# Kernel optimization log

Measured on AMD Instinct MI355X. Metric: run time of the kernel, lower is better.

The kernel has to match this reference:

```python
import jax, jax.numpy as jnp
import numpy as np


def setup_inputs() -> dict:
    key = jax.random.key(0)
    k1, k2 = jax.random.split(key)
    inputs = jax.random.normal(k1, (16, 64, 64, 512), dtype=jnp.float32)
    gamma = jax.random.normal(k2, (1,), dtype=jnp.float32)
    return {"inputs": inputs, "gamma": gamma}


def reference(inputs, gamma):
    # inputs: [B, H, W, C] (NHWC), gamma: [1]
    b, h, w, c = inputs.shape
    vec_a = inputs.reshape(b, h * w, c)           # [B, HW, C]
    # channel-channel Gram matrix: [B, C, C]
    aTa = jnp.einsum('bnc,bnd->bcd', vec_a, vec_a)
    softmax_aTa = jax.nn.softmax(aTa, axis=-1)     # softmax over last channel axis
    # attend over channels: [B, HW, C] @ [B, C, C] -> [B, HW, C]
    aaTa = jnp.einsum('bnc,bcd->bnd', vec_a, softmax_aTa)
    aaTa = aaTa.reshape(b, h, w, c)
    return gamma * aaTa + inputs
```

## Files before the change

kernel.cpp:

```cpp
#include <hip/hip_runtime.h>
#include <stdint.h>

#define BB 16
#define NN 4096
#define CC 512
#define PELEM ((size_t)BB * CC * CC)

typedef __attribute__((ext_vector_type(8))) short bf16x8;
typedef __attribute__((ext_vector_type(4))) float f32x4;

__device__ __forceinline__ unsigned short to_bf16(float f) {
  unsigned int u = __float_as_uint(f);
  u += 0x7fffu + ((u >> 16) & 1u);
  return (unsigned short)(u >> 16);
}
__device__ __forceinline__ float bf16_to_f32(unsigned short h) {
  return __uint_as_float(((unsigned int)h) << 16);
}

__device__ __forceinline__ void gload_lds16(const void* g, void* l) {
  __builtin_amdgcn_global_load_lds(
      (const __attribute__((address_space(1))) unsigned int*)g,
      (__attribute__((address_space(3))) unsigned int*)l, 16, 0, 0);
}

template <int RS, int KLEN>
__device__ __forceinline__ void nt_gemm(const unsigned short* __restrict__ aB,
                                        const unsigned short* __restrict__ bB,
                                        f32x4 acc[4][4],
                                        unsigned short* lA, unsigned short* lB) {
  const int tid  = threadIdx.x;
  const int wid  = tid >> 6;
  const int lane = tid & 63;
  const int wr   = (wid >> 1) * 64;
  const int wc   = (wid & 1) * 64;

  const f32x4 zero = {0.f, 0.f, 0.f, 0.f};
#pragma unroll
  for (int i = 0; i < 4; ++i)
#pragma unroll
    for (int j = 0; j < 4; ++j) acc[i][j] = zero;

  const int srow = lane >> 3;
  const int gsrc = (lane & 7) ^ srow;

#pragma unroll 1
  for (int k0 = 0; k0 < KLEN; k0 += 64) {
#pragma unroll
    for (int i = 0; i < 4; ++i) {
      const int issue = wid * 4 + i;
      const int row   = issue * 8 + srow;
      const size_t go = (size_t)row * RS + k0 + gsrc * 8;
      gload_lds16(aB + go, lA + issue * 512);
      gload_lds16(bB + go, lB + issue * 512);
    }
    __syncthreads();

#pragma unroll
    for (int s = 0; s < 2; ++s) {
      bf16x8 af[4], bfr[4];
#pragma unroll
      for (int mf = 0; mf < 4; ++mf) {
        const int row = wr + mf * 16 + (lane & 15);
        const int ch  = (s * 4 + (lane >> 4)) ^ (row & 7);
        af[mf] = *(const bf16x8*)(lA + row * 64 + ch * 8);
      }
#pragma unroll
      for (int nf = 0; nf < 4; ++nf) {
        const int row = wc + nf * 16 + (lane & 15);
        const int ch  = (s * 4 + (lane >> 4)) ^ (row & 7);
        bfr[nf] = *(const bf16x8*)(lB + row * 64 + ch * 8);
      }
#pragma unroll
      for (int mf = 0; mf < 4; ++mf)
#pragma unroll
        for (int nf = 0; nf < 4; ++nf)
          acc[mf][nf] = __builtin_amdgcn_mfma_f32_16x16x32_bf16(
              af[mf], bfr[nf], acc[mf][nf], 0, 0, 0);
    }
    __syncthreads();
  }
}

__global__ __launch_bounds__(256) void k_convert(const float* __restrict__ in,
                                                 unsigned short* __restrict__ a16,
                                                 unsigned short* __restrict__ at16) {
  __shared__ unsigned short lt[64][68];
  const int b  = blockIdx.y;
  const int tn = blockIdx.x >> 3, tc = blockIdx.x & 7;
  const int n0 = tn * 64, c0 = tc * 64;
  const float* src = in + ((size_t)b * NN + n0) * CC + c0;
  unsigned short* adst = a16 + ((size_t)b * NN + n0) * CC + c0;

#pragma unroll
  for (int i = 0; i < 4; ++i) {
    const int id = i * 256 + threadIdx.x;
    const int n = id >> 4, ch = id & 15;
    float4 v = *(const float4*)(src + (size_t)n * CC + ch * 4);
    ushort4 o;
    o.x = to_bf16(v.x); o.y = to_bf16(v.y); o.z = to_bf16(v.z); o.w = to_bf16(v.w);
    *(ushort4*)(adst + (size_t)n * CC + ch * 4) = o;
    lt[ch * 4 + 0][n] = o.x;
    lt[ch * 4 + 1][n] = o.y;
    lt[ch * 4 + 2][n] = o.z;
    lt[ch * 4 + 3][n] = o.w;
  }
  __syncthreads();
  unsigned short* tdst = at16 + ((size_t)b * CC + c0) * NN + n0;
#pragma unroll
  for (int i = 0; i < 4; ++i) {
    const int id = i * 256 + threadIdx.x;
    const int c = id >> 4, ch2 = id & 15;
    uint2 w = *(const uint2*)&lt[c][ch2 * 4];
    *(uint2*)(tdst + (size_t)c * NN + ch2 * 4) = w;
  }
}

__global__ __launch_bounds__(256) void k_gram(const unsigned short* __restrict__ at,
                                              float* __restrict__ parts) {
  __shared__ __align__(16) unsigned short lA[128 * 64];
  __shared__ __align__(16) unsigned short lB[128 * 64];
  const int bid  = blockIdx.x;
  const int work = (bid & 7) * 128 + (bid >> 3);
  const int b    = work >> 6;
  const int r    = work & 63;
  const int ks   = r >> 4;
  const int tile = r & 15;
  const int c0 = (tile & 3) * 128;
  const int d0 = (tile >> 2) * 128;
  const unsigned short* aB = at + ((size_t)b * CC + c0) * NN + ks * 1024;
  const unsigned short* bB = at + ((size_t)b * CC + d0) * NN + ks * 1024;
  f32x4 acc[4][4];
  nt_gemm<NN, 1024>(aB, bB, acc, lA, lB);

  const int lane = threadIdx.x & 63, wid = threadIdx.x >> 6;
  const int wr = (wid >> 1) * 64, wc = (wid & 1) * 64;
  float* gb = parts + (size_t)ks * PELEM + (size_t)b * CC * CC;
#pragma unroll
  for (int mf = 0; mf < 4; ++mf)
#pragma unroll
    for (int nf = 0; nf < 4; ++nf)
#pragma unroll
      for (int q = 0; q < 4; ++q) {
        const int row = c0 + wr + mf * 16 + (lane >> 4) * 4 + q;
        const int col = d0 + wc + nf * 16 + (lane & 15);
        gb[(size_t)row * CC + col] = acc[mf][nf][q];
      }
}

__global__ __launch_bounds__(256) void k_softmax(const float* __restrict__ parts,
                                                 unsigned short* __restrict__ st) {
  __shared__ unsigned short ls[32][512];
  const int b  = blockIdx.x >> 4;
  const int cb = blockIdx.x & 15;
  const int wid = threadIdx.x >> 6, lane = threadIdx.x & 63;

#pragma unroll 1
  for (int i = 0; i < 8; ++i) {
    const int rl = wid * 8 + i;
    const int c  = cb * 32 + rl;
    const int r7 = rl & 7;
    const float* base = parts + ((size_t)b * CC + c) * CC;
    float4 v0 = {0.f, 0.f, 0.f, 0.f}, v1 = {0.f, 0.f, 0.f, 0.f};
#pragma unroll
    for (int p = 0; p < 4; ++p) {
      float4 a = *(const float4*)(base + (size_t)p * PELEM + lane * 4);
      float4 bq = *(const float4*)(base + (size_t)p * PELEM + 256 + lane * 4);
      v0.x += a.x; v0.y += a.y; v0.z += a.z; v0.w += a.w;
      v1.x += bq.x; v1.y += bq.y; v1.z += bq.z; v1.w += bq.w;
    }
    float m = fmaxf(fmaxf(fmaxf(v0.x, v0.y), fmaxf(v0.z, v0.w)),
                    fmaxf(fmaxf(v1.x, v1.y), fmaxf(v1.z, v1.w)));
#pragma unroll
    for (int off = 32; off > 0; off >>= 1) m = fmaxf(m, __shfl_xor(m, off));
    float e0 = expf(v0.x - m), e1 = expf(v0.y - m), e2 = expf(v0.z - m), e3 = expf(v0.w - m);
    float e4 = expf(v1.x - m), e5 = expf(v1.y - m), e6 = expf(v1.z - m), e7 = expf(v1.w - m);
    float s = e0 + e1 + e2 + e3 + e4 + e5 + e6 + e7;
#pragma unroll
    for (int off = 32; off > 0; off >>= 1) s += __shfl_xor(s, off);
    const float pinv = 1.0f / s;
    ushort4 o0, o1;
    o0.x = to_bf16(e0 * pinv); o0.y = to_bf16(e1 * pinv);
    o0.z = to_bf16(e2 * pinv); o0.w = to_bf16(e3 * pinv);
    o1.x = to_bf16(e4 * pinv); o1.y = to_bf16(e5 * pinv);
    o1.z = to_bf16(e6 * pinv); o1.w = to_bf16(e7 * pinv);
    *(ushort4*)&ls[rl][(lane ^ r7) << 2]         = o0;
    *(ushort4*)&ls[rl][256 + ((lane ^ r7) << 2)] = o1;
  }
  __syncthreads();

#pragma unroll 1
  for (int i = 0; i < 2; ++i) {
    const int d = i * 256 + threadIdx.x;
    unsigned int u[16];
#pragma unroll
    for (int k = 0; k < 16; ++k) {
      const int c0i = 2 * k, c1i = 2 * k + 1;
      const unsigned int lo = ls[c0i][(((d >> 2) ^ (c0i & 7)) << 2) | (d & 3)];
      const unsigned int hi = ls[c1i][(((d >> 2) ^ (c1i & 7)) << 2) | (d & 3)];
      u[k] = lo | (hi << 16);
    }
    unsigned short* dst = st + ((size_t)b * CC + d) * CC + cb * 32;
    uint4 w0 = {u[0], u[1], u[2], u[3]};
    uint4 w1 = {u[4], u[5], u[6], u[7]};
    uint4 w2 = {u[8], u[9], u[10], u[11]};
    uint4 w3 = {u[12], u[13], u[14], u[15]};
    *(uint4*)(dst + 0)  = w0;
    *(uint4*)(dst + 8)  = w1;
    *(uint4*)(dst + 16) = w2;
    *(uint4*)(dst + 24) = w3;
  }
}

__global__ __launch_bounds__(256) void k_out(const unsigned short* __restrict__ a16,
                                             const unsigned short* __restrict__ st,
                                             const float* __restrict__ gammap,
                                             float* __restrict__ outp) {
  __shared__ __align__(16) unsigned short lA[128 * 64];
  __shared__ __align__(16) unsigned short lB[128 * 64];
  const int bid  = blockIdx.x;
  const int work = (bid & 7) * 256 + (bid >> 3);
  const int b    = work >> 7;
  const int r    = work & 127;
  const int nt   = r >> 5;
  const int mt   = r & 31;
  const int n0 = mt * 128, d0 = nt * 128;
  const unsigned short* aB = a16 + ((size_t)b * NN + n0) * CC;
  const unsigned short* bB = st + ((size_t)b * CC + d0) * CC;
  f32x4 acc[4][4];
  nt_gemm<CC, CC>(aB, bB, acc, lA, lB);

  const float g = gammap[0];
  const int lane = threadIdx.x & 63, wid = threadIdx.x >> 6;
  const int wr = (wid >> 1) * 64, wc = (wid & 1) * 64;
  const unsigned short* xr = a16 + ((size_t)b * NN + n0) * CC + d0;
  float* ob = outp + ((size_t)b * NN + n0) * CC + d0;
#pragma unroll
  for (int mf = 0; mf < 4; ++mf)
#pragma unroll
    for (int nf = 0; nf < 4; ++nf)
#pragma unroll
      for (int q = 0; q < 4; ++q) {
        const int row = wr + mf * 16 + (lane >> 4) * 4 + q;
        const int col = wc + nf * 16 + (lane & 15);
        const size_t off = (size_t)row * CC + col;
        ob[off] = fmaf(g, acc[mf][nf][q], bf16_to_f32(xr[off]));
      }
}

extern "C" void kernel_launch(void* const* d_in, const int* in_sizes, int n_in,
                              void* d_out, int out_size, void* d_ws, size_t ws_size,
                              hipStream_t stream) {
  const float* in    = (const float*)d_in[0];
  const float* gamma = (const float*)d_in[1];
  float* outp = (float*)d_out;

  unsigned short* a16  = (unsigned short*)d_ws;
  unsigned short* stb  = (unsigned short*)((char*)d_ws + ((size_t)64 << 20));
  unsigned short* at16 = (unsigned short*)d_out;
  float*          parts = (float*)((char*)d_out + ((size_t)64 << 20));

  k_convert<<<dim3(512, 16), 256, 0, stream>>>(in, a16, at16);
  k_gram<<<dim3(1024), 256, 0, stream>>>(at16, parts);
  k_softmax<<<dim3(256), 256, 0, stream>>>(parts, stb);
  k_out<<<dim3(2048), 256, 0, stream>>>(a16, stb, gamma, outp);
}
```

Before: 370.7 us.

## Double-buffer GEMM LDS tiles, exploit Gram symmetry, and vectorize transpose in convert

The shared NT GEMM now uses two LDS buffers so the next k-tile's global-to-LDS loads are issued before computing the current tile, overlapping memory with MFMA work. The Gram kernel computes only upper-triangular 128x128 tiles (10 of 16 per batch and k-split) and writes the mirrored tile through an LDS transpose, cutting Gram launches from 1024 to 640 blocks. The convert kernel is restructured so each thread transposes a 4x4 block in registers and writes wider LDS and global stores. Double buffering doubles LDS per block to 64KB, which may reduce occupancy, and the mirrored write adds extra stores and syncs.

```diff
diff --git a/kernel.cpp b/kernel.cpp
--- a/kernel.cpp
+++ b/kernel.cpp
@@ -28,7 +28,7 @@
 __device__ __forceinline__ void nt_gemm(const unsigned short* __restrict__ aB,
                                         const unsigned short* __restrict__ bB,
                                         f32x4 acc[4][4],
-                                        unsigned short* lA, unsigned short* lB) {
+                                        unsigned short* lds) {
   const int tid  = threadIdx.x;
   const int wid  = tid >> 6;
   const int lane = tid & 63;
@@ -43,19 +43,21 @@
 
   const int srow = lane >> 3;
   const int gsrc = (lane & 7) ^ srow;
-
-#pragma unroll 1
-  for (int k0 = 0; k0 < KLEN; k0 += 64) {
+  constexpr int NT = KLEN / 64;
+
+  auto stage = [&](int bf, int k0) {
 #pragma unroll
     for (int i = 0; i < 4; ++i) {
       const int issue = wid * 4 + i;
       const int row   = issue * 8 + srow;
       const size_t go = (size_t)row * RS + k0 + gsrc * 8;
-      gload_lds16(aB + go, lA + issue * 512);
-      gload_lds16(bB + go, lB + issue * 512);
-    }
-    __syncthreads();
-
+      gload_lds16(aB + go, lds + bf * 16384 + issue * 512);
+      gload_lds16(bB + go, lds + bf * 16384 + 8192 + issue * 512);
+    }
+  };
+  auto compute = [&](int bf) {
+    const unsigned short* lA = lds + bf * 16384;
+    const unsigned short* lB = lA + 8192;
 #pragma unroll
     for (int s = 0; s < 2; ++s) {
       bf16x8 af[4], bfr[4];
@@ -78,64 +80,86 @@
           acc[mf][nf] = __builtin_amdgcn_mfma_f32_16x16x32_bf16(
               af[mf], bfr[nf], acc[mf][nf], 0, 0, 0);
     }
+  };
+
+  stage(0, 0);
+  __syncthreads();
+  int cur = 0;
+#pragma unroll 1
+  for (int t = 0; t < NT; ++t) {
+    if (t + 1 < NT) stage(cur ^ 1, (t + 1) * 64);
+    compute(cur);
     __syncthreads();
+    cur ^= 1;
   }
 }
 
 __global__ __launch_bounds__(256) void k_convert(const float* __restrict__ in,
                                                  unsigned short* __restrict__ a16,
                                                  unsigned short* __restrict__ at16) {
-  __shared__ unsigned short lt[64][68];
+  __shared__ unsigned short lt[64 * 68];
   const int b  = blockIdx.y;
   const int tn = blockIdx.x >> 3, tc = blockIdx.x & 7;
   const int n0 = tn * 64, c0 = tc * 64;
-  const float* src = in + ((size_t)b * NN + n0) * CC + c0;
-  unsigned short* adst = a16 + ((size_t)b * NN + n0) * CC + c0;
-
-#pragma unroll
-  for (int i = 0; i < 4; ++i) {
-    const int id = i * 256 + threadIdx.x;
-    const int n = id >> 4, ch = id & 15;
-    float4 v = *(const float4*)(src + (size_t)n * CC + ch * 4);
-    ushort4 o;
-    o.x = to_bf16(v.x); o.y = to_bf16(v.y); o.z = to_bf16(v.z); o.w = to_bf16(v.w);
-    *(ushort4*)(adst + (size_t)n * CC + ch * 4) = o;
-    lt[ch * 4 + 0][n] = o.x;
-    lt[ch * 4 + 1][n] = o.y;
-    lt[ch * 4 + 2][n] = o.z;
-    lt[ch * 4 + 3][n] = o.w;
+  const int t   = threadIdx.x;
+  const int ctc = t & 15;
+  const int ntq = t >> 4;
+
+  const float* src = in + ((size_t)b * NN + n0 + 4 * ntq) * CC + c0 + 4 * ctc;
+  unsigned short* adst = a16 + ((size_t)b * NN + n0 + 4 * ntq) * CC + c0 + 4 * ctc;
+
+  unsigned short ob[4][4];
+#pragma unroll
+  for (int j = 0; j < 4; ++j) {
+    float4 v = *(const float4*)(src + (size_t)j * CC);
+    ob[j][0] = to_bf16(v.x); ob[j][1] = to_bf16(v.y);
+    ob[j][2] = to_bf16(v.z); ob[j][3] = to_bf16(v.w);
+    ushort4 o = {ob[j][0], ob[j][1], ob[j][2], ob[j][3]};
+    *(ushort4*)(adst + (size_t)j * CC) = o;
+  }
+#pragma unroll
+  for (int q = 0; q < 4; ++q) {
+    ushort4 w = {ob[0][q], ob[1][q], ob[2][q], ob[3][q]};
+    *(ushort4*)&lt[(4 * ctc + q) * 68 + 4 * ntq] = w;
   }
   __syncthreads();
-  unsigned short* tdst = at16 + ((size_t)b * CC + c0) * NN + n0;
-#pragma unroll
-  for (int i = 0; i < 4; ++i) {
-    const int id = i * 256 + threadIdx.x;
-    const int c = id >> 4, ch2 = id & 15;
-    uint2 w = *(const uint2*)&lt[c][ch2 * 4];
-    *(uint2*)(tdst + (size_t)c * NN + ch2 * 4) = w;
-  }
+
+  const int c_l = t >> 2, w4 = t & 3;
+  const unsigned short* lr = lt + c_l * 68;
+  uint2 r0a = *(const uint2*)(lr + 8 * w4);
+  uint2 r0b = *(const uint2*)(lr + 8 * w4 + 4);
+  uint2 r1a = *(const uint2*)(lr + 8 * w4 + 32);
+  uint2 r1b = *(const uint2*)(lr + 8 * w4 + 36);
+  unsigned short* tb = at16 + ((size_t)b * CC + c0 + c_l) * NN + n0;
+  uint4 s0 = {r0a.x, r0a.y, r0b.x, r0b.y};
+  uint4 s1 = {r1a.x, r1a.y, r1b.x, r1b.y};
+  *(uint4*)(tb + 8 * w4)      = s0;
+  *(uint4*)(tb + 8 * w4 + 32) = s1;
 }
 
 __global__ __launch_bounds__(256) void k_gram(const unsigned short* __restrict__ at,
                                               float* __restrict__ parts) {
-  __shared__ __align__(16) unsigned short lA[128 * 64];
-  __shared__ __align__(16) unsigned short lB[128 * 64];
+  __shared__ __align__(16) unsigned short lds[32768];
   const int bid  = blockIdx.x;
-  const int work = (bid & 7) * 128 + (bid >> 3);
-  const int b    = work >> 6;
-  const int r    = work & 63;
-  const int ks   = r >> 4;
-  const int tile = r & 15;
-  const int c0 = (tile & 3) * 128;
-  const int d0 = (tile >> 2) * 128;
+  const int work = (bid & 7) * 80 + (bid >> 3);
+  const int b    = work / 40;
+  const int r    = work % 40;
+  const int ks   = r / 10;
+  const int t10  = r % 10;
+  const int ti = t10 < 4 ? 0 : t10 < 7 ? 1 : t10 < 9 ? 2 : 3;
+  const int tj = t10 < 4 ? t10 : t10 < 7 ? t10 - 3 : t10 < 9 ? t10 - 5 : 3;
+  const int c0 = ti * 128, d0 = tj * 128;
+
   const unsigned short* aB = at + ((size_t)b * CC + c0) * NN + ks * 1024;
   const unsigned short* bB = at + ((size_t)b * CC + d0) * NN + ks * 1024;
   f32x4 acc[4][4];
-  nt_gemm<NN, 1024>(aB, bB, acc, lA, lB);
-
-  const int lane = threadIdx.x & 63, wid = threadIdx.x >> 6;
+  nt_gemm<NN, 1024>(aB, bB, acc, lds);
+
+  const int tid = threadIdx.x;
+  const int lane = tid & 63, wid = tid >> 6;
   const int wr = (wid >> 1) * 64, wc = (wid & 1) * 64;
   float* gb = parts + (size_t)ks * PELEM + (size_t)b * CC * CC;
+
 #pragma unroll
   for (int mf = 0; mf < 4; ++mf)
 #pragma unroll
@@ -146,6 +170,38 @@
         const int col = d0 + wc + nf * 16 + (lane & 15);
         gb[(size_t)row * CC + col] = acc[mf][nf][q];
       }
+
+  if (c0 != d0) {
+    float* sf = (float*)lds;
+#pragma unroll 1
+    for (int h = 0; h < 2; ++h) {
+      __syncthreads();
+      if ((wid >> 1) == h) {
+#pragma unroll
+        for (int mf = 0; mf < 4; ++mf)
+#pragma unroll
+          for (int nf = 0; nf < 4; ++nf)
+#pragma unroll
+            for (int q = 0; q < 4; ++q) {
+              const int row_l = mf * 16 + (lane >> 4) * 4 + q;
+              const int col   = wc + nf * 16 + (lane & 15);
+              sf[row_l * 132 + col] = acc[mf][nf][q];
+            }
+      }
+      __syncthreads();
+      const int d_l = tid >> 1;
+      const int rh  = tid & 1;
+      float vals[32];
+#pragma unroll
+      for (int u = 0; u < 32; ++u) vals[u] = sf[(32 * rh + u) * 132 + d_l];
+      float* dst = gb + (size_t)(d0 + d_l) * CC + c0 + 64 * h + 32 * rh;
+#pragma unroll
+      for (int s = 0; s < 8; ++s) {
+        float4 w = {vals[4 * s], vals[4 * s + 1], vals[4 * s + 2], vals[4 * s + 3]};
+        *(float4*)(dst + 4 * s) = w;
+      }
+    }
+  }
 }
 
 __global__ __launch_bounds__(256) void k_softmax(const float* __restrict__ parts,
@@ -216,8 +272,7 @@
                                              const unsigned short* __restrict__ st,
                                              const float* __restrict__ gammap,
                                              float* __restrict__ outp) {
-  __shared__ __align__(16) unsigned short lA[128 * 64];
-  __shared__ __align__(16) unsigned short lB[128 * 64];
+  __shared__ __align__(16) unsigned short lds[32768];
   const int bid  = blockIdx.x;
   const int work = (bid & 7) * 256 + (bid >> 3);
   const int b    = work >> 7;
@@ -228,7 +283,7 @@
   const unsigned short* aB = a16 + ((size_t)b * NN + n0) * CC;
   const unsigned short* bB = st + ((size_t)b * CC + d0) * CC;
   f32x4 acc[4][4];
-  nt_gemm<CC, CC>(aB, bB, acc, lA, lB);
+  nt_gemm<CC, CC>(aB, bB, acc, lds);
 
   const float g = gammap[0];
   const int lane = threadIdx.x & 63, wid = threadIdx.x >> 6;
@@ -261,7 +316,7 @@
   float*          parts = (float*)((char*)d_out + ((size_t)64 << 20));
 
   k_convert<<<dim3(512, 16), 256, 0, stream>>>(in, a16, at16);
-  k_gram<<<dim3(1024), 256, 0, stream>>>(at16, parts);
+  k_gram<<<dim3(640), 256, 0, stream>>>(at16, parts);
   k_softmax<<<dim3(256), 256, 0, stream>>>(parts, stb);
   k_out<<<dim3(2048), 256, 0, stream>>>(a16, stb, gamma, outp);
 }
```

After: 356.7 us. 3.8% less time.
